# Performance work log

Hardware: AMD Instinct MI355X
Metric: run time of the kernel (lower is better)

Reference implementation:

```python
import jax, jax.numpy as jnp
import numpy as np

N, C, K2 = 40000, 128, 9  # active voxels, channels, 3x3 kernel taps
HEAD_OUT = {"hm": 3, "center": 2, "center_z": 1, "dim": 3, "rot": 2}
EPS = 1e-5
INIT_BIAS = -2.66


def setup_inputs() -> dict:
    key = jax.random.key(0)
    ks = jax.random.split(key, 16)
    feats = jax.random.normal(ks[0], (N, C), dtype=jnp.float32)
    # precomputed submanifold-conv neighbor indices (one per kernel tap, all valid)
    nbr_idx = jax.random.randint(ks[1], (N, K2), 0, N, dtype=jnp.int32)
    H = len(HEAD_OUT)
    inp = {"feats": feats, "nbr_idx": nbr_idx}
    # stacked 3x3 SubMConv weights for all heads (kaiming-ish scale)
    inp["W1"] = jax.random.normal(ks[2], (H, K2, C, C), dtype=jnp.float32) * (2.0 / (K2 * C)) ** 0.5
    inp["gamma"] = jnp.ones((H, C), jnp.float32)
    inp["beta"] = jnp.zeros((H, C), jnp.float32)
    for i, (name, oc) in enumerate(HEAD_OUT.items()):
        inp[f"w_{name}"] = jax.random.normal(ks[3 + i], (C, oc), dtype=jnp.float32) * (2.0 / C) ** 0.5
        inp[f"b_{name}"] = (jnp.full((oc,), INIT_BIAS, jnp.float32) if name == "hm"
                             else jnp.zeros((oc,), jnp.float32))
    return inp


def reference(feats, nbr_idx, W1, gamma, beta,
              w_hm, b_hm, w_center, b_center, w_center_z, b_center_z,
              w_dim, b_dim, w_rot, b_rot):
    # SubMConv2d as gather + contraction over kernel taps (shared by all heads)
    gathered = feats[nbr_idx]                       # [N, K2, C]
    y = jnp.einsum('nkc,hkcd->hnd', gathered, W1)   # [H, N, C]
    # BatchNorm1d (training-mode forward: biased batch stats over voxels) + ReLU
    mean = y.mean(axis=1, keepdims=True)
    var = y.var(axis=1, keepdims=True)
    y = jax.nn.relu((y - mean) * jax.lax.rsqrt(var + EPS) * gamma[:, None, :] + beta[:, None, :])
    # per-head 1x1 SubMConv with bias
    heads = [(w_hm, b_hm), (w_center, b_center), (w_center_z, b_center_z),
             (w_dim, b_dim), (w_rot, b_rot)]
    outs = [y[i] @ w + b for i, (w, b) in enumerate(heads)]
    # concat head outputs along channel: [N, 3+2+1+3+2] = [N, 11]
    return jnp.concatenate(outs, axis=-1)
```

## Files before the change

kernel.cpp:

```cpp
#include <hip/hip_runtime.h>
#include <stdint.h>

#define NVOX 40000
#define CCH  128
#define K2   9
#define NH   5
#define TILES 313

typedef __attribute__((ext_vector_type(8))) short bf16x8;
typedef __attribute__((ext_vector_type(4))) float f32x4;

__device__ __forceinline__ unsigned short f2b(float f) {
  union { float f; unsigned int u; } v; v.f = f;
  return (unsigned short)((v.u + 0x7fffu + ((v.u >> 16) & 1u)) >> 16);
}
__device__ __forceinline__ float b2f(unsigned short u) {
  union { unsigned int u; float f; } v; v.u = ((unsigned int)u) << 16;
  return v.f;
}
__device__ __forceinline__ void g2l16(const void* g, void* l) {
  __builtin_amdgcn_global_load_lds(
      (const __attribute__((address_space(1))) unsigned int*)g,
      (__attribute__((address_space(3))) unsigned int*)l, 16, 0, 0);
}
__device__ __forceinline__ int swz(int row, int col) {
  return row * 128 + ((((col >> 3) ^ (row & 15)) << 3) | (col & 7));
}

__global__ void prep(const float4* __restrict__ feats, ushort4* __restrict__ fb,
                     const float* __restrict__ w1, unsigned short* __restrict__ w1t) {
  __shared__ unsigned short t[128 * 34];
  int b = blockIdx.x;
  if (b < 5000) {
    int i = b * 256 + threadIdx.x;
    if (i < NVOX * CCH / 4) {
      float4 v = feats[i];
      ushort4 r;
      r.x = f2b(v.x); r.y = f2b(v.y); r.z = f2b(v.z); r.w = f2b(v.w);
      fb[i] = r;
    }
    return;
  }
  int bb = b - 5000;
  int tile = bb >> 2;
  int q = bb & 3;
  const float* src = w1 + (size_t)tile * 16384 + q * 32 * 128;
  for (int e = threadIdx.x; e < 4096; e += 256) {
    int c = e >> 7, d = e & 127;
    t[d * 34 + c] = f2b(src[e]);
  }
  __syncthreads();
  unsigned short* dst = w1t + (size_t)tile * 16384 + q * 32;
  for (int e = threadIdx.x; e < 4096; e += 256) {
    int d = e >> 5, c = e & 31;
    dst[d * 128 + c] = t[d * 34 + c];
  }
}

__global__ void __launch_bounds__(256, 3) conv_gemm(
    const unsigned short* __restrict__ fb,
    const int* __restrict__ nbr,
    const unsigned short* __restrict__ w1t,
    unsigned short* __restrict__ yb,
    float* __restrict__ sums)
{
  __shared__ unsigned short As[128 * 128];
  __shared__ int idxs[128 * K2];

  const int bid = blockIdx.x;
  const int s = bid / 40;
  const int r = bid % 40;
  const int h = r >> 3;
  const int x = r & 7;
  const int tile = s * 8 + x;
  if (tile >= TILES) return;
  const int n0 = tile * 128;

  const int tid = threadIdx.x;
  const int wave = tid >> 6;
  const int lane = tid & 63;
  const int lrow = lane >> 4;
  const int lcol = lane & 15;
  const int wm = wave >> 1, wn = wave & 1;

  for (int i = tid; i < 128 * K2; i += 256) {
    int rr = i / K2;
    int kk = i - rr * K2;
    int gn = n0 + rr; if (gn > NVOX - 1) gn = NVOX - 1;
    idxs[i] = nbr[gn * K2 + kk];
  }
  __syncthreads();

  f32x4 acc[4][4] = {};

  {
    int ridx[8];
#pragma unroll
    for (int i = 0; i < 8; ++i)
      ridx[i] = idxs[(wave * 32 + i * 4 + lrow) * K2 + 0];
#pragma unroll
    for (int i = 0; i < 8; ++i) {
      int row = wave * 32 + i * 4 + lrow;
      g2l16(fb + (size_t)ridx[i] * CCH + ((lcol ^ (row & 15)) << 3),
            &As[(wave * 32 + i * 4) * CCH]);
    }
  }

  for (int k = 0; k < K2; ++k) {
    const unsigned short* wp = w1t + (((size_t)h * K2 + k) << 14);
    __syncthreads();

#pragma unroll
    for (int kc = 0; kc < 4; ++kc) {
      bf16x8 af[4], bfr[4];
#pragma unroll
      for (int ni = 0; ni < 4; ++ni) {
        int row = wn * 64 + ni * 16 + lcol;
        bfr[ni] = *(const bf16x8*)(wp + row * CCH + kc * 32 + lrow * 8);
      }
#pragma unroll
      for (int mi = 0; mi < 4; ++mi) {
        int row = wm * 64 + mi * 16 + lcol;
        af[mi] = *(const bf16x8*)&As[row * CCH + (((kc * 4 + lrow) ^ (row & 15)) << 3)];
      }
#pragma unroll
      for (int mi = 0; mi < 4; ++mi)
#pragma unroll
        for (int ni = 0; ni < 4; ++ni)
          acc[mi][ni] = __builtin_amdgcn_mfma_f32_16x16x32_bf16(af[mi], bfr[ni], acc[mi][ni], 0, 0, 0);
    }
    __syncthreads();

    if (k + 1 < K2) {
      int ridx[8];
#pragma unroll
      for (int i = 0; i < 8; ++i)
        ridx[i] = idxs[(wave * 32 + i * 4 + lrow) * K2 + k + 1];
#pragma unroll
      for (int i = 0; i < 8; ++i) {
        int row = wave * 32 + i * 4 + lrow;
        g2l16(fb + (size_t)ridx[i] * CCH + ((lcol ^ (row & 15)) << 3),
              &As[(wave * 32 + i * 4) * CCH]);
      }
    }
  }

#pragma unroll
  for (int mi = 0; mi < 4; ++mi)
#pragma unroll
    for (int ni = 0; ni < 4; ++ni)
#pragma unroll
      for (int rr = 0; rr < 4; ++rr) {
        int row = wm * 64 + mi * 16 + lrow * 4 + rr;
        int col = wn * 64 + ni * 16 + lcol;
        As[swz(row, col)] = f2b(acc[mi][ni][rr]);
      }
  __syncthreads();

  for (int i = tid; i < 2048; i += 256) {
    int row = i >> 4;
    int c = i & 15;
    if (n0 + row < NVOX)
      *(bf16x8*)(yb + ((size_t)h * NVOX + n0 + row) * CCH + c * 8) =
          *(const bf16x8*)&As[row * 128 + ((c ^ (row & 15)) << 3)];
  }

  {
    int col = tid & 127, half = tid >> 7;
    int rbase = half * 64;
    int nvalid = NVOX - n0 - rbase;
    if (nvalid > 64) nvalid = 64;
    float sm = 0.f, q = 0.f;
    for (int rr = 0; rr < nvalid; ++rr) {
      float z = b2f(As[swz(rbase + rr, col)]);
      sm += z; q += z * z;
    }
    if (nvalid > 0) {
      atomicAdd(&sums[h * CCH + col], sm);
      atomicAdd(&sums[NH * CCH + h * CCH + col], q);
    }
  }
}

__global__ void finalize_bn(const float* __restrict__ sums, const float* __restrict__ gamma,
                            const float* __restrict__ beta, float* __restrict__ ssb) {
  int h = blockIdx.x, c = threadIdx.x;
  float mean = sums[h * CCH + c] * (1.f / NVOX);
  float var = sums[NH * CCH + h * CCH + c] * (1.f / NVOX) - mean * mean;
  float rstd = rsqrtf(var + 1e-5f);
  float scale = rstd * gamma[h * CCH + c];
  ssb[h * CCH + c] = scale;
  ssb[NH * CCH + h * CCH + c] = beta[h * CCH + c] - mean * scale;
}

__global__ void __launch_bounds__(256) head_fuse(
    const unsigned short* __restrict__ yb, const float* __restrict__ ssb,
    const float* __restrict__ w_hm, const float* __restrict__ b_hm,
    const float* __restrict__ w_ce, const float* __restrict__ b_ce,
    const float* __restrict__ w_cz, const float* __restrict__ b_cz,
    const float* __restrict__ w_dm, const float* __restrict__ b_dm,
    const float* __restrict__ w_rt, const float* __restrict__ b_rt,
    float* __restrict__ out)
{
  int t = blockIdx.x * 256 + threadIdx.x;
  if (t >= NH * NVOX) return;
  int h = t / NVOX;
  int v = t - h * NVOX;

  const float* wp; const float* bp; int oc, off;
  switch (h) {
    case 0: wp = w_hm; bp = b_hm; oc = 3; off = 0; break;
    case 1: wp = w_ce; bp = b_ce; oc = 2; off = 3; break;
    case 2: wp = w_cz; bp = b_cz; oc = 1; off = 5; break;
    case 3: wp = w_dm; bp = b_dm; oc = 3; off = 6; break;
    default: wp = w_rt; bp = b_rt; oc = 2; off = 9; break;
  }
  float a0 = bp[0];
  float a1 = (oc > 1) ? bp[1] : 0.f;
  float a2 = (oc > 2) ? bp[2] : 0.f;

  const bf16x8* yp = (const bf16x8*)(yb + ((size_t)h * NVOX + v) * CCH);
  const float* sc = ssb + h * CCH;
  const float* sh = ssb + NH * CCH + h * CCH;

  for (int q8 = 0; q8 < 16; ++q8) {
    bf16x8 pk = yp[q8];
#pragma unroll
    for (int e = 0; e < 8; ++e) {
      int d = q8 * 8 + e;
      float z = fmaf(b2f((unsigned short)pk[e]), sc[d], sh[d]);
      z = fmaxf(z, 0.f);
      const float* wr = wp + d * oc;
      a0 = fmaf(z, wr[0], a0);
      if (oc > 1) a1 = fmaf(z, wr[1], a1);
      if (oc > 2) a2 = fmaf(z, wr[2], a2);
    }
  }
  float* op = out + (size_t)v * 11 + off;
  op[0] = a0;
  if (oc > 1) op[1] = a1;
  if (oc > 2) op[2] = a2;
}

extern "C" void kernel_launch(void* const* d_in, const int* in_sizes, int n_in,
                              void* d_out, int out_size, void* d_ws, size_t ws_size,
                              hipStream_t stream) {
  const float* feats = (const float*)d_in[0];
  const int*   nbr   = (const int*)d_in[1];
  const float* W1    = (const float*)d_in[2];
  const float* gamma = (const float*)d_in[3];
  const float* beta  = (const float*)d_in[4];
  const float* w_hm = (const float*)d_in[5];  const float* b_hm = (const float*)d_in[6];
  const float* w_ce = (const float*)d_in[7];  const float* b_ce = (const float*)d_in[8];
  const float* w_cz = (const float*)d_in[9];  const float* b_cz = (const float*)d_in[10];
  const float* w_dm = (const float*)d_in[11]; const float* b_dm = (const float*)d_in[12];
  const float* w_rt = (const float*)d_in[13]; const float* b_rt = (const float*)d_in[14];
  float* out = (float*)d_out;

  char* ws = (char*)d_ws;
  unsigned short* w1t = (unsigned short*)ws;
  unsigned short* fb  = (unsigned short*)(ws + 11796480);
  unsigned short* yb  = (unsigned short*)(ws + 22036480);
  float* sums = (float*)(ws + 73236480);
  float* ssb  = (float*)(ws + 73241600);

  hipMemsetAsync(sums, 0, 2 * NH * CCH * sizeof(float), stream);
  prep<<<5180, 256, 0, stream>>>((const float4*)feats, (ushort4*)fb, W1, w1t);
  conv_gemm<<<1600, 256, 0, stream>>>(fb, nbr, w1t, yb, sums);
  finalize_bn<<<NH, CCH, 0, stream>>>(sums, gamma, beta, ssb);
  head_fuse<<<782, 256, 0, stream>>>(yb, ssb, w_hm, b_hm, w_ce, b_ce, w_cz, b_cz,
                                     w_dm, b_dm, w_rt, b_rt, out);
}
```

Before: 286.3 us.

## Stage weights in double-buffered LDS, read gathered rows directly, restructure head kernel

The conv GEMM now stages the per-tap weight tile into double-buffered shared memory with async global-to-LDS loads, prefetching the next tap while the current one computes. Gathered feature rows are read directly from global memory into registers instead of through LDS. Occupancy is lowered to two blocks per CU to fit the larger LDS footprint. The head kernel now processes 64 voxels per block across all five heads, stages rows through swizzled LDS, reduces partial sums in shared memory and writes each output row once. The aim is to cut uncoalesced per-thread row reads and redundant weight fetches, at the cost of lower occupancy and uncached gather latency on the A operand.

```diff
diff --git a/kernel.cpp b/kernel.cpp
--- a/kernel.cpp
+++ b/kernel.cpp
@@ -57,14 +57,25 @@
   }
 }
 
-__global__ void __launch_bounds__(256, 3) conv_gemm(
+__device__ __forceinline__ void stageB(unsigned short* dstbuf, const unsigned short* wp,
+                                       int wave, int lane) {
+  int lcol = lane & 15, lrow = lane >> 4;
+#pragma unroll
+  for (int i = 0; i < 8; ++i) {
+    int elem = wave * 4096 + i * 512;
+    int row = (elem >> 7) + lrow;
+    g2l16(wp + row * 128 + ((lcol ^ (row & 15)) << 3), &dstbuf[elem]);
+  }
+}
+
+__global__ void __launch_bounds__(256, 2) conv_gemm(
     const unsigned short* __restrict__ fb,
     const int* __restrict__ nbr,
     const unsigned short* __restrict__ w1t,
     unsigned short* __restrict__ yb,
     float* __restrict__ sums)
 {
-  __shared__ unsigned short As[128 * 128];
+  __shared__ unsigned short Bs[2][128 * 128];
   __shared__ int idxs[128 * K2];
 
   const int bid = blockIdx.x;
@@ -79,8 +90,8 @@
   const int tid = threadIdx.x;
   const int wave = tid >> 6;
   const int lane = tid & 63;
-  const int lrow = lane >> 4;
-  const int lcol = lane & 15;
+  const int m = lane & 15;
+  const int quad = lane >> 4;
   const int wm = wave >> 1, wn = wave & 1;
 
   for (int i = tid; i < 128 * K2; i += 256) {
@@ -89,39 +100,38 @@
     int gn = n0 + rr; if (gn > NVOX - 1) gn = NVOX - 1;
     idxs[i] = nbr[gn * K2 + kk];
   }
+
+  stageB(Bs[0], w1t + (((size_t)h * K2 + 0) << 14), wave, lane);
   __syncthreads();
 
   f32x4 acc[4][4] = {};
 
-  {
-    int ridx[8];
-#pragma unroll
-    for (int i = 0; i < 8; ++i)
-      ridx[i] = idxs[(wave * 32 + i * 4 + lrow) * K2 + 0];
-#pragma unroll
-    for (int i = 0; i < 8; ++i) {
-      int row = wave * 32 + i * 4 + lrow;
-      g2l16(fb + (size_t)ridx[i] * CCH + ((lcol ^ (row & 15)) << 3),
-            &As[(wave * 32 + i * 4) * CCH]);
-    }
-  }
-
   for (int k = 0; k < K2; ++k) {
-    const unsigned short* wp = w1t + (((size_t)h * K2 + k) << 14);
+    asm volatile("s_waitcnt vmcnt(0)" ::: "memory");
     __syncthreads();
+
+    if (k + 1 < K2)
+      stageB(Bs[(k + 1) & 1], w1t + (((size_t)h * K2 + k + 1) << 14), wave, lane);
+
+    const unsigned short* Bcur = Bs[k & 1];
+
+    const unsigned short* aptr[4];
+#pragma unroll
+    for (int mi = 0; mi < 4; ++mi) {
+      int rowA = idxs[(wm * 64 + mi * 16 + m) * K2 + k];
+      aptr[mi] = fb + (size_t)rowA * CCH + quad * 8;
+    }
 
 #pragma unroll
     for (int kc = 0; kc < 4; ++kc) {
       bf16x8 af[4], bfr[4];
 #pragma unroll
+      for (int mi = 0; mi < 4; ++mi)
+        af[mi] = *(const bf16x8*)(aptr[mi] + kc * 32);
+#pragma unroll
       for (int ni = 0; ni < 4; ++ni) {
-        int row = wn * 64 + ni * 16 + lcol;
-        bfr[ni] = *(const bf16x8*)(wp + row * CCH + kc * 32 + lrow * 8);
-      }
-#pragma unroll
-      for (int mi = 0; mi < 4; ++mi) {
-        int row = wm * 64 + mi * 16 + lcol;
-        af[mi] = *(const bf16x8*)&As[row * CCH + (((kc * 4 + lrow) ^ (row & 15)) << 3)];
+        int row = wn * 64 + ni * 16 + m;
+        bfr[ni] = *(const bf16x8*)&Bcur[row * CCH + (((kc * 4 + quad) ^ (row & 15)) << 3)];
       }
 #pragma unroll
       for (int mi = 0; mi < 4; ++mi)
@@ -129,31 +139,18 @@
         for (int ni = 0; ni < 4; ++ni)
           acc[mi][ni] = __builtin_amdgcn_mfma_f32_16x16x32_bf16(af[mi], bfr[ni], acc[mi][ni], 0, 0, 0);
     }
-    __syncthreads();
-
-    if (k + 1 < K2) {
-      int ridx[8];
-#pragma unroll
-      for (int i = 0; i < 8; ++i)
-        ridx[i] = idxs[(wave * 32 + i * 4 + lrow) * K2 + k + 1];
-#pragma unroll
-      for (int i = 0; i < 8; ++i) {
-        int row = wave * 32 + i * 4 + lrow;
-        g2l16(fb + (size_t)ridx[i] * CCH + ((lcol ^ (row & 15)) << 3),
-              &As[(wave * 32 + i * 4) * CCH]);
-      }
-    }
-  }
-
+  }
+
+  unsigned short* epi = Bs[1];
 #pragma unroll
   for (int mi = 0; mi < 4; ++mi)
 #pragma unroll
     for (int ni = 0; ni < 4; ++ni)
 #pragma unroll
       for (int rr = 0; rr < 4; ++rr) {
-        int row = wm * 64 + mi * 16 + lrow * 4 + rr;
-        int col = wn * 64 + ni * 16 + lcol;
-        As[swz(row, col)] = f2b(acc[mi][ni][rr]);
+        int row = wm * 64 + mi * 16 + quad * 4 + rr;
+        int col = wn * 64 + ni * 16 + m;
+        epi[swz(row, col)] = f2b(acc[mi][ni][rr]);
       }
   __syncthreads();
 
@@ -162,7 +159,7 @@
     int c = i & 15;
     if (n0 + row < NVOX)
       *(bf16x8*)(yb + ((size_t)h * NVOX + n0 + row) * CCH + c * 8) =
-          *(const bf16x8*)&As[row * 128 + ((c ^ (row & 15)) << 3)];
+          *(const bf16x8*)&epi[row * 128 + ((c ^ (row & 15)) << 3)];
   }
 
   {
@@ -172,7 +169,7 @@
     if (nvalid > 64) nvalid = 64;
     float sm = 0.f, q = 0.f;
     for (int rr = 0; rr < nvalid; ++rr) {
-      float z = b2f(As[swz(rbase + rr, col)]);
+      float z = b2f(epi[swz(rbase + rr, col)]);
       sm += z; q += z * z;
     }
     if (nvalid > 0) {
@@ -202,44 +199,74 @@
     const float* __restrict__ w_rt, const float* __restrict__ b_rt,
     float* __restrict__ out)
 {
-  int t = blockIdx.x * 256 + threadIdx.x;
-  if (t >= NH * NVOX) return;
-  int h = t / NVOX;
-  int v = t - h * NVOX;
-
-  const float* wp; const float* bp; int oc, off;
-  switch (h) {
-    case 0: wp = w_hm; bp = b_hm; oc = 3; off = 0; break;
-    case 1: wp = w_ce; bp = b_ce; oc = 2; off = 3; break;
-    case 2: wp = w_cz; bp = b_cz; oc = 1; off = 5; break;
-    case 3: wp = w_dm; bp = b_dm; oc = 3; off = 6; break;
-    default: wp = w_rt; bp = b_rt; oc = 2; off = 9; break;
-  }
-  float a0 = bp[0];
-  float a1 = (oc > 1) ? bp[1] : 0.f;
-  float a2 = (oc > 2) ? bp[2] : 0.f;
-
-  const bf16x8* yp = (const bf16x8*)(yb + ((size_t)h * NVOX + v) * CCH);
-  const float* sc = ssb + h * CCH;
-  const float* sh = ssb + NH * CCH + h * CCH;
-
-  for (int q8 = 0; q8 < 16; ++q8) {
-    bf16x8 pk = yp[q8];
-#pragma unroll
-    for (int e = 0; e < 8; ++e) {
-      int d = q8 * 8 + e;
-      float z = fmaf(b2f((unsigned short)pk[e]), sc[d], sh[d]);
-      z = fmaxf(z, 0.f);
-      const float* wr = wp + d * oc;
-      a0 = fmaf(z, wr[0], a0);
-      if (oc > 1) a1 = fmaf(z, wr[1], a1);
-      if (oc > 2) a2 = fmaf(z, wr[2], a2);
-    }
-  }
-  float* op = out + (size_t)v * 11 + off;
-  op[0] = a0;
-  if (oc > 1) op[1] = a1;
-  if (oc > 2) op[2] = a2;
+  __shared__ unsigned short t[64 * 128];
+  __shared__ float pbuf[4][64][12];
+
+  const int tid = threadIdx.x;
+  const int v0 = blockIdx.x * 64;
+  const int vx = tid & 63;
+  const int qd = tid >> 6;
+
+  float part[11];
+#pragma unroll
+  for (int j = 0; j < 11; ++j) part[j] = 0.f;
+
+#pragma unroll
+  for (int h = 0; h < NH; ++h) {
+    __syncthreads();
+#pragma unroll
+    for (int i = 0; i < 4; ++i) {
+      int idx = i * 256 + tid;
+      int row = idx >> 4, c = idx & 15;
+      *(bf16x8*)&t[row * 128 + ((c ^ (row & 15)) << 3)] =
+          *(const bf16x8*)(yb + ((size_t)h * NVOX + v0 + row) * CCH + c * 8);
+    }
+    __syncthreads();
+
+    const float* sc = ssb + h * CCH;
+    const float* sh = ssb + NH * CCH + h * CCH;
+    const float* wp; int oc, off;
+    switch (h) {
+      case 0: wp = w_hm; oc = 3; off = 0; break;
+      case 1: wp = w_ce; oc = 2; off = 3; break;
+      case 2: wp = w_cz; oc = 1; off = 5; break;
+      case 3: wp = w_dm; oc = 3; off = 6; break;
+      default: wp = w_rt; oc = 2; off = 9; break;
+    }
+#pragma unroll
+    for (int qq = 0; qq < 4; ++qq) {
+      int q8 = qd * 4 + qq;
+      bf16x8 pk = *(const bf16x8*)&t[vx * 128 + ((q8 ^ (vx & 15)) << 3)];
+#pragma unroll
+      for (int e = 0; e < 8; ++e) {
+        int d = q8 * 8 + e;
+        float z = fmaf(b2f((unsigned short)pk[e]), sc[d], sh[d]);
+        z = fmaxf(z, 0.f);
+        const float* wr = wp + d * oc;
+        part[off] = fmaf(z, wr[0], part[off]);
+        if (oc > 1) part[off + 1] = fmaf(z, wr[1], part[off + 1]);
+        if (oc > 2) part[off + 2] = fmaf(z, wr[2], part[off + 2]);
+      }
+    }
+  }
+
+#pragma unroll
+  for (int j = 0; j < 11; ++j) pbuf[qd][vx][j] = part[j];
+  __syncthreads();
+  if (tid < 64) {
+    float o[11];
+#pragma unroll
+    for (int j = 0; j < 11; ++j)
+      o[j] = pbuf[0][tid][j] + pbuf[1][tid][j] + pbuf[2][tid][j] + pbuf[3][tid][j];
+    o[0] += b_hm[0]; o[1] += b_hm[1]; o[2] += b_hm[2];
+    o[3] += b_ce[0]; o[4] += b_ce[1];
+    o[5] += b_cz[0];
+    o[6] += b_dm[0]; o[7] += b_dm[1]; o[8] += b_dm[2];
+    o[9] += b_rt[0]; o[10] += b_rt[1];
+    float* op = out + (size_t)(v0 + tid) * 11;
+#pragma unroll
+    for (int j = 0; j < 11; ++j) op[j] = o[j];
+  }
 }
 
 extern "C" void kernel_launch(void* const* d_in, const int* in_sizes, int n_in,
@@ -268,6 +295,6 @@
   prep<<<5180, 256, 0, stream>>>((const float4*)feats, (ushort4*)fb, W1, w1t);
   conv_gemm<<<1600, 256, 0, stream>>>(fb, nbr, w1t, yb, sums);
   finalize_bn<<<NH, CCH, 0, stream>>>(sums, gamma, beta, ssb);
-  head_fuse<<<782, 256, 0, stream>>>(yb, ssb, w_hm, b_hm, w_ce, b_ce, w_cz, b_cz,
+  head_fuse<<<625, 256, 0, stream>>>(yb, ssb, w_hm, b_hm, w_ce, b_ce, w_cz, b_cz,
                                      w_dm, b_dm, w_rt, b_rt, out);
 }
```

New measurement: 293.1 us. 1.02x slower.
